# Kernel optimization log

Measured on AMD Instinct MI355X. Metric: run time of the kernel, lower is better.

Reference implementation:

```python
import jax, jax.numpy as jnp
import numpy as np

N, D_IN, UNITS = 8192, 4096, 4096

def ste_sign(k):
    # larq ste_sign forward: sign with sign(0) -> +1
    return jnp.where(k >= 0, 1.0, -1.0).astype(k.dtype)

def setup_inputs() -> dict:
    key = jax.random.key(0)
    kx, kk = jax.random.split(key)
    x = jax.random.normal(kx, (N, D_IN), dtype=jnp.float32)
    kernel = jax.random.normal(kk, (D_IN, UNITS), dtype=jnp.float32)
    return {"x": x, "kernel": kernel}

def reference(x, kernel):
    # y = x @ sign(kernel); the `+ reduce_sum(x)*0` in the original is a no-op
    return x @ ste_sign(kernel)
```

## Files before the change

kernel.cpp:

```cpp
#include <hip/hip_runtime.h>
#include <stdint.h>

typedef __attribute__((ext_vector_type(8))) __bf16 bf16x8;
typedef __attribute__((ext_vector_type(4))) float f32x4;

__device__ inline unsigned short f32_to_bf16_rne(float f) {
  union { float f; uint32_t u; } c; c.f = f;
  uint32_t u = c.u;
  uint32_t r = (u + 0x7FFFu + ((u >> 16) & 1u)) >> 16;
  return (unsigned short)r;
}

__global__ __launch_bounds__(256) void convert_x_kernel(const float* __restrict__ X,
                                                        unsigned short* __restrict__ A,
                                                        size_t n) {
  size_t i = (size_t)blockIdx.x * 256 + threadIdx.x;
  size_t stride = (size_t)gridDim.x * 256;
  for (size_t e = i * 4; e < n; e += stride * 4) {
    const float4 v = *reinterpret_cast<const float4*>(X + e);
    ushort4 o;
    o.x = f32_to_bf16_rne(v.x);
    o.y = f32_to_bf16_rne(v.y);
    o.z = f32_to_bf16_rne(v.z);
    o.w = f32_to_bf16_rne(v.w);
    *reinterpret_cast<ushort4*>(A + e) = o;
  }
}

__global__ __launch_bounds__(256) void sign_transpose_kernel(const float* __restrict__ Km,
                                                             unsigned short* __restrict__ Bt,
                                                             int K, int N) {
  __shared__ unsigned short tile[64][65];
  const int k0 = blockIdx.x * 64;
  const int n0 = blockIdx.y * 64;
  const int t = threadIdx.x;
#pragma unroll
  for (int i = 0; i < 16; ++i) {
    int idx = t + i * 256;
    int kk = idx >> 6, nn = idx & 63;
    float v = Km[(size_t)(k0 + kk) * N + (n0 + nn)];
    tile[kk][nn] = (v >= 0.0f) ? (unsigned short)0x3F80u : (unsigned short)0xBF80u;
  }
  __syncthreads();
#pragma unroll
  for (int i = 0; i < 16; ++i) {
    int idx = t + i * 256;
    int nn = idx >> 6, kk = idx & 63;
    Bt[(size_t)(n0 + nn) * K + (k0 + kk)] = tile[kk][nn];
  }
}


__device__ __forceinline__ void stage_mat(const unsigned short* __restrict__ G,
                                          size_t grow0, int K, int k0,
                                          unsigned short* lds_wave_base,
                                          int tid) {
#pragma unroll
  for (int i = 0; i < 2; ++i) {
    const int row = i * 128 + (tid >> 2);
    const int srcslot = (tid & 3) ^ ((row >> 1) & 3);
    const unsigned short* ga = G + (grow0 + row) * (size_t)K + k0 + srcslot * 8;
    __builtin_amdgcn_global_load_lds(
        (const __attribute__((address_space(1))) void*)ga,
        (__attribute__((address_space(3))) void*)(lds_wave_base + i * 4096),
        16, 0, 0);
  }
}

#define MFMA8(ACCR, AFRAG, BFRAG, I0, I1)                                             \
  __builtin_amdgcn_s_setprio(1);                                                     \
  _Pragma("unroll")                                                                   \
  for (int mi = (I0); mi < (I1); ++mi)                                                \
    _Pragma("unroll")                                                                 \
    for (int ni = 0; ni < 4; ++ni)                                                    \
      acc[(ACCR) + mi][ni] = __builtin_amdgcn_mfma_f32_16x16x32_bf16(                 \
          AFRAG[mi], BFRAG[ni], acc[(ACCR) + mi][ni], 0, 0, 0);                       \
  __builtin_amdgcn_s_setprio(0);                                                      \
  __builtin_amdgcn_sched_barrier(0);

#define GEMM_ITER(T, AFC, BFC, AFN, BFN)                                              \
  {                                                                                   \
    const int cb = ((T) & 3) * 16384;                                                 \
    const int ts = ((T) + 3 < NTt) ? ((T) + 3) : (NTt - 1);                           \
    const int tb = (ts & 3) * 16384;                                                  \
    const int nb = ((T) + 1 < NTt) ? ((((T) + 1) & 3) * 16384) : cb;                  \
    bf16x8 af1[4];                                                                    \
                                                \
    _Pragma("unroll")                                                                 \
    for (int mi = 0; mi < 4; ++mi)                                                    \
      af1[mi] = *reinterpret_cast<const bf16x8*>(&lds[cb + aoff + 2048 + mi * 512]);  \
    stage_mat(A, a_row0, K, ts * 32, &lds[tb + wv * 512], tid);                       \
    __builtin_amdgcn_sched_barrier(0);                                                \
    MFMA8(0, AFC, BFC, 0, 2)                                                          \
                                                       \
    _Pragma("unroll")                                                                 \
    for (int ni = 0; ni < 2; ++ni)                                                    \
      BFN[ni] = *reinterpret_cast<const bf16x8*>(&lds[nb + boff + ni * 512]);         \
    __builtin_amdgcn_sched_barrier(0);                                                \
    MFMA8(0, AFC, BFC, 2, 4)                                                          \
                                \
    _Pragma("unroll")                                                                 \
    for (int ni = 2; ni < 4; ++ni)                                                    \
      BFN[ni] = *reinterpret_cast<const bf16x8*>(&lds[nb + boff + ni * 512]);         \
    _Pragma("unroll")                                                                 \
    for (int mi = 0; mi < 2; ++mi)                                                    \
      AFN[mi] = *reinterpret_cast<const bf16x8*>(&lds[nb + aoff + mi * 512]);         \
    stage_mat(Bt, b_row0, K, ts * 32, &lds[tb + 8192 + wv * 512], tid);               \
    __builtin_amdgcn_sched_barrier(0);                                                \
    MFMA8(4, af1, BFC, 0, 2)                                                          \
                                                       \
    _Pragma("unroll")                                                                 \
    for (int mi = 2; mi < 4; ++mi)                                                    \
      AFN[mi] = *reinterpret_cast<const bf16x8*>(&lds[nb + aoff + mi * 512]);         \
    __builtin_amdgcn_sched_barrier(0);                                                \
    MFMA8(4, af1, BFC, 2, 4)                                                          \
    asm volatile("s_waitcnt vmcnt(4)\n" ::: "memory");                                \
    __builtin_amdgcn_s_barrier();                                                     \
  }

__global__ __launch_bounds__(512, 2) void gemm_bf16_256(const unsigned short* __restrict__ A,
                                                        const unsigned short* __restrict__ Bt,
                                                        float* __restrict__ C,
                                                        int M, int N, int K) {
  __shared__ unsigned short lds[4 * 16384];

  const int nBN = N >> 8;
  const int nwg = gridDim.x;
  const int bid = blockIdx.x;
  int swz = bid;
  if ((nwg & 7) == 0) {
    const int q = nwg >> 3;
    swz = (bid & 7) * q + (bid >> 3);
  }
  const size_t a_row0 = (size_t)(swz / nBN) * 256;
  const size_t b_row0 = (size_t)(swz % nBN) * 256;

  const int tid = threadIdx.x;
  const int wv = tid >> 6, ln = tid & 63;
  const int llo = ln & 15, lhi = ln >> 4;
  const int wr = wv >> 2, wc = wv & 3;
  const int sA = lhi ^ ((llo >> 1) & 3);

  const int aoff = (wr * 128 + llo) * 32 + sA * 8;
  const int boff = 8192 + (wc * 64 + llo) * 32 + sA * 8;

  const int NTt = K >> 5;

  f32x4 acc[8][4];
#pragma unroll
  for (int i = 0; i < 8; ++i)
#pragma unroll
    for (int j = 0; j < 4; ++j) acc[i][j] = (f32x4){0.f, 0.f, 0.f, 0.f};

#pragma unroll
  for (int tt = 0; tt < 3; ++tt) {
    stage_mat(A, a_row0, K, tt * 32, &lds[tt * 16384 + wv * 512], tid);
    stage_mat(Bt, b_row0, K, tt * 32, &lds[tt * 16384 + 8192 + wv * 512], tid);
  }
  asm volatile("s_waitcnt vmcnt(4)\n" ::: "memory");
  __builtin_amdgcn_s_barrier();

  bf16x8 af0_a[4], bfr_a[4], af0_b[4], bfr_b[4];
#pragma unroll
  for (int ni = 0; ni < 4; ++ni)
    bfr_a[ni] = *reinterpret_cast<const bf16x8*>(&lds[boff + ni * 512]);
#pragma unroll
  for (int mi = 0; mi < 4; ++mi)
    af0_a[mi] = *reinterpret_cast<const bf16x8*>(&lds[aoff + mi * 512]);

  for (int t = 0; t < NTt; t += 2) {
    GEMM_ITER(t, af0_a, bfr_a, af0_b, bfr_b)
    GEMM_ITER(t + 1, af0_b, bfr_b, af0_a, bfr_a)
  }

#pragma unroll
  for (int mi = 0; mi < 8; ++mi) {
#pragma unroll
    for (int ni = 0; ni < 4; ++ni) {
      const size_t col = b_row0 + wc * 64 + ni * 16 + llo;
      const size_t rbase = a_row0 + wr * 128 + mi * 16 + lhi * 4;
#pragma unroll
      for (int j = 0; j < 4; ++j)
        C[(rbase + j) * (size_t)N + col] = acc[mi][ni][j];
    }
  }
}

__global__ __launch_bounds__(256) void gemm_f32_fallback(const float* __restrict__ X,
                                                         const float* __restrict__ Km,
                                                         float* __restrict__ C,
                                                         int M, int N, int K) {
  __shared__ float As[64][16];
  __shared__ float Bs[16][65];
  const int nBN = N / 64;
  const int bm = blockIdx.x / nBN;
  const int bn = blockIdx.x % nBN;
  const int t = threadIdx.x;
  const int tx = t & 15, ty = t >> 4;
  float acc[4][4] = {};
  for (int kb = 0; kb < K; kb += 16) {
#pragma unroll
    for (int i = 0; i < 4; ++i) {
      int e = t + i * 256;
      int r = e >> 4, c = e & 15;
      As[r][c] = X[(size_t)(bm * 64 + r) * K + kb + c];
      int rk = e >> 6, cn = e & 63;
      float v = Km[(size_t)(kb + rk) * N + bn * 64 + cn];
      Bs[rk][cn] = (v >= 0.f) ? 1.f : -1.f;
    }
    __syncthreads();
#pragma unroll
    for (int kk = 0; kk < 16; ++kk) {
      float a[4], b[4];
#pragma unroll
      for (int r = 0; r < 4; ++r) a[r] = As[ty * 4 + r][kk];
#pragma unroll
      for (int c = 0; c < 4; ++c) b[c] = Bs[kk][tx * 4 + c];
#pragma unroll
      for (int r = 0; r < 4; ++r)
#pragma unroll
        for (int c = 0; c < 4; ++c) acc[r][c] += a[r] * b[c];
    }
    __syncthreads();
  }
#pragma unroll
  for (int r = 0; r < 4; ++r)
#pragma unroll
    for (int c = 0; c < 4; ++c)
      C[(size_t)(bm * 64 + ty * 4 + r) * N + bn * 64 + tx * 4 + c] = acc[r][c];
}

extern "C" void kernel_launch(void* const* d_in, const int* in_sizes, int n_in,
                              void* d_out, int out_size, void* d_ws, size_t ws_size,
                              hipStream_t stream) {
  const float* x = (const float*)d_in[0];
  const float* kern = (const float*)d_in[1];
  float* out = (float*)d_out;

  const int K = 4096;
  const int N = 4096;
  const int M = in_sizes[0] / K;

  const size_t a_bytes = (size_t)M * K * 2;
  const size_t b_bytes = (size_t)N * K * 2;

  if (ws_size >= a_bytes + b_bytes && (M % 256) == 0 && (N % 256) == 0 && (K % 128) == 0) {
    unsigned short* A = (unsigned short*)d_ws;
    unsigned short* Bt = (unsigned short*)((char*)d_ws + a_bytes);
    convert_x_kernel<<<2048, 256, 0, stream>>>(x, A, (size_t)M * K);
    sign_transpose_kernel<<<dim3(K / 64, N / 64), 256, 0, stream>>>(kern, Bt, K, N);
    gemm_bf16_256<<<(M / 256) * (N / 256), 512, 0, stream>>>(A, Bt, out, M, N, K);
  } else {
    gemm_f32_fallback<<<(M / 64) * (N / 64), 256, 0, stream>>>(x, kern, out, M, N, K);
  }
}
```

Measured before the change: 272.2 us.

## Shrink GEMM tile to 128x256 with 4 waves and triple-buffered LDS

Replaces the 256x256, 8-wave GEMM block with a 128x256, 4-wave block where each wave owns all 128 rows and a 64-column strip. The pipeline drops from a 4-stage to a 3-stage LDS ring with rotating buffer offsets and a prefetch distance of two, and it waits for all loads (vmcnt(0)) at each step. The intent is a smaller LDS footprint and more workgroups for occupancy and load balance. The cost is lower data reuse per block, twice as many blocks re-reading B, and a shallower load overlap.

```diff
diff --git a/kernel.cpp b/kernel.cpp
--- a/kernel.cpp
+++ b/kernel.cpp
@@ -51,24 +51,25 @@
 }
 
 
-__device__ __forceinline__ void stage_mat(const unsigned short* __restrict__ G,
-                                          size_t grow0, int K, int k0,
-                                          unsigned short* lds_wave_base,
-                                          int tid) {
-#pragma unroll
-  for (int i = 0; i < 2; ++i) {
-    const int row = i * 128 + (tid >> 2);
+template <int NISS>
+__device__ __forceinline__ void stage_rows(const unsigned short* __restrict__ G,
+                                           size_t grow0, int K, int k0,
+                                           unsigned short* lds_base,
+                                           int tid) {
+#pragma unroll
+  for (int i = 0; i < NISS; ++i) {
+    const int row = i * 64 + (tid >> 2);
     const int srcslot = (tid & 3) ^ ((row >> 1) & 3);
     const unsigned short* ga = G + (grow0 + row) * (size_t)K + k0 + srcslot * 8;
     __builtin_amdgcn_global_load_lds(
         (const __attribute__((address_space(1))) void*)ga,
-        (__attribute__((address_space(3))) void*)(lds_wave_base + i * 4096),
+        (__attribute__((address_space(3))) void*)(lds_base + i * 2048 + (tid >> 6) * 512),
         16, 0, 0);
   }
 }
 
 #define MFMA8(ACCR, AFRAG, BFRAG, I0, I1)                                             \
-  __builtin_amdgcn_s_setprio(1);                                                     \
+  __builtin_amdgcn_s_setprio(1);                                                      \
   _Pragma("unroll")                                                                   \
   for (int mi = (I0); mi < (I1); ++mi)                                                \
     _Pragma("unroll")                                                                 \
@@ -78,51 +79,44 @@
   __builtin_amdgcn_s_setprio(0);                                                      \
   __builtin_amdgcn_sched_barrier(0);
 
-#define GEMM_ITER(T, AFC, BFC, AFN, BFN)                                              \
+#define GEMM_ITER(T, CBo, NBo, TBo, AFC, BFC, AFN, BFN)                               \
   {                                                                                   \
-    const int cb = ((T) & 3) * 16384;                                                 \
-    const int ts = ((T) + 3 < NTt) ? ((T) + 3) : (NTt - 1);                           \
-    const int tb = (ts & 3) * 16384;                                                  \
-    const int nb = ((T) + 1 < NTt) ? ((((T) + 1) & 3) * 16384) : cb;                  \
+    const int ts = ((T) + 2 < NTt) ? ((T) + 2) : (NTt - 1);                           \
     bf16x8 af1[4];                                                                    \
-                                                \
     _Pragma("unroll")                                                                 \
     for (int mi = 0; mi < 4; ++mi)                                                    \
-      af1[mi] = *reinterpret_cast<const bf16x8*>(&lds[cb + aoff + 2048 + mi * 512]);  \
-    stage_mat(A, a_row0, K, ts * 32, &lds[tb + wv * 512], tid);                       \
+      af1[mi] = *reinterpret_cast<const bf16x8*>(&lds[(CBo) + aoff + 2048 + mi * 512]); \
+    stage_rows<2>(A, a_row0, K, ts * 32, (unsigned short*)lds + (TBo), tid);          \
     __builtin_amdgcn_sched_barrier(0);                                                \
     MFMA8(0, AFC, BFC, 0, 2)                                                          \
-                                                       \
     _Pragma("unroll")                                                                 \
     for (int ni = 0; ni < 2; ++ni)                                                    \
-      BFN[ni] = *reinterpret_cast<const bf16x8*>(&lds[nb + boff + ni * 512]);         \
+      BFN[ni] = *reinterpret_cast<const bf16x8*>(&lds[(NBo) + boff + ni * 512]);      \
     __builtin_amdgcn_sched_barrier(0);                                                \
     MFMA8(0, AFC, BFC, 2, 4)                                                          \
-                                \
     _Pragma("unroll")                                                                 \
     for (int ni = 2; ni < 4; ++ni)                                                    \
-      BFN[ni] = *reinterpret_cast<const bf16x8*>(&lds[nb + boff + ni * 512]);         \
+      BFN[ni] = *reinterpret_cast<const bf16x8*>(&lds[(NBo) + boff + ni * 512]);      \
     _Pragma("unroll")                                                                 \
     for (int mi = 0; mi < 2; ++mi)                                                    \
-      AFN[mi] = *reinterpret_cast<const bf16x8*>(&lds[nb + aoff + mi * 512]);         \
-    stage_mat(Bt, b_row0, K, ts * 32, &lds[tb + 8192 + wv * 512], tid);               \
+      AFN[mi] = *reinterpret_cast<const bf16x8*>(&lds[(NBo) + aoff + mi * 512]);      \
+    stage_rows<4>(Bt, b_row0, K, ts * 32, (unsigned short*)lds + (TBo) + 4096, tid);  \
     __builtin_amdgcn_sched_barrier(0);                                                \
     MFMA8(4, af1, BFC, 0, 2)                                                          \
-                                                       \
     _Pragma("unroll")                                                                 \
     for (int mi = 2; mi < 4; ++mi)                                                    \
-      AFN[mi] = *reinterpret_cast<const bf16x8*>(&lds[nb + aoff + mi * 512]);         \
+      AFN[mi] = *reinterpret_cast<const bf16x8*>(&lds[(NBo) + aoff + mi * 512]);      \
     __builtin_amdgcn_sched_barrier(0);                                                \
     MFMA8(4, af1, BFC, 2, 4)                                                          \
-    asm volatile("s_waitcnt vmcnt(4)\n" ::: "memory");                                \
+    asm volatile("s_waitcnt vmcnt(0)\n" ::: "memory");                                \
     __builtin_amdgcn_s_barrier();                                                     \
   }
 
-__global__ __launch_bounds__(512, 2) void gemm_bf16_256(const unsigned short* __restrict__ A,
-                                                        const unsigned short* __restrict__ Bt,
-                                                        float* __restrict__ C,
-                                                        int M, int N, int K) {
-  __shared__ unsigned short lds[4 * 16384];
+__global__ __launch_bounds__(256, 2) void gemm_bf16_128x256(const unsigned short* __restrict__ A,
+                                                            const unsigned short* __restrict__ Bt,
+                                                            float* __restrict__ C,
+                                                            int M, int N, int K) {
+  __shared__ unsigned short lds[3 * 12288];
 
   const int nBN = N >> 8;
   const int nwg = gridDim.x;
@@ -132,17 +126,17 @@
     const int q = nwg >> 3;
     swz = (bid & 7) * q + (bid >> 3);
   }
-  const size_t a_row0 = (size_t)(swz / nBN) * 256;
+  const size_t a_row0 = (size_t)(swz / nBN) * 128;
   const size_t b_row0 = (size_t)(swz % nBN) * 256;
 
   const int tid = threadIdx.x;
   const int wv = tid >> 6, ln = tid & 63;
   const int llo = ln & 15, lhi = ln >> 4;
-  const int wr = wv >> 2, wc = wv & 3;
+  const int wc = wv;
   const int sA = lhi ^ ((llo >> 1) & 3);
 
-  const int aoff = (wr * 128 + llo) * 32 + sA * 8;
-  const int boff = 8192 + (wc * 64 + llo) * 32 + sA * 8;
+  const int aoff = llo * 32 + sA * 8;
+  const int boff = 4096 + (wc * 64 + llo) * 32 + sA * 8;
 
   const int NTt = K >> 5;
 
@@ -152,12 +146,11 @@
 #pragma unroll
     for (int j = 0; j < 4; ++j) acc[i][j] = (f32x4){0.f, 0.f, 0.f, 0.f};
 
-#pragma unroll
-  for (int tt = 0; tt < 3; ++tt) {
-    stage_mat(A, a_row0, K, tt * 32, &lds[tt * 16384 + wv * 512], tid);
-    stage_mat(Bt, b_row0, K, tt * 32, &lds[tt * 16384 + 8192 + wv * 512], tid);
-  }
-  asm volatile("s_waitcnt vmcnt(4)\n" ::: "memory");
+  stage_rows<2>(A, a_row0, K, 0, (unsigned short*)lds, tid);
+  stage_rows<4>(Bt, b_row0, K, 0, (unsigned short*)lds + 4096, tid);
+  stage_rows<2>(A, a_row0, K, 32, (unsigned short*)lds + 12288, tid);
+  stage_rows<4>(Bt, b_row0, K, 32, (unsigned short*)lds + 12288 + 4096, tid);
+  asm volatile("s_waitcnt vmcnt(0)\n" ::: "memory");
   __builtin_amdgcn_s_barrier();
 
   bf16x8 af0_a[4], bfr_a[4], af0_b[4], bfr_b[4];
@@ -168,9 +161,12 @@
   for (int mi = 0; mi < 4; ++mi)
     af0_a[mi] = *reinterpret_cast<const bf16x8*>(&lds[aoff + mi * 512]);
 
+  int cb = 0, nb2 = 12288, tb = 24576;
   for (int t = 0; t < NTt; t += 2) {
-    GEMM_ITER(t, af0_a, bfr_a, af0_b, bfr_b)
-    GEMM_ITER(t + 1, af0_b, bfr_b, af0_a, bfr_a)
+    GEMM_ITER(t, cb, nb2, tb, af0_a, bfr_a, af0_b, bfr_b)
+    { int tmp = cb; cb = nb2; nb2 = tb; tb = tmp; }
+    GEMM_ITER(t + 1, cb, nb2, tb, af0_b, bfr_b, af0_a, bfr_a)
+    { int tmp = cb; cb = nb2; nb2 = tb; tb = tmp; }
   }
 
 #pragma unroll
@@ -178,7 +174,7 @@
 #pragma unroll
     for (int ni = 0; ni < 4; ++ni) {
       const size_t col = b_row0 + wc * 64 + ni * 16 + llo;
-      const size_t rbase = a_row0 + wr * 128 + mi * 16 + lhi * 4;
+      const size_t rbase = a_row0 + mi * 16 + lhi * 4;
 #pragma unroll
       for (int j = 0; j < 4; ++j)
         C[(rbase + j) * (size_t)N + col] = acc[mi][ni][j];
@@ -244,12 +240,12 @@
   const size_t a_bytes = (size_t)M * K * 2;
   const size_t b_bytes = (size_t)N * K * 2;
 
-  if (ws_size >= a_bytes + b_bytes && (M % 256) == 0 && (N % 256) == 0 && (K % 128) == 0) {
+  if (ws_size >= a_bytes + b_bytes && (M % 128) == 0 && (N % 256) == 0 && (K % 128) == 0) {
     unsigned short* A = (unsigned short*)d_ws;
     unsigned short* Bt = (unsigned short*)((char*)d_ws + a_bytes);
     convert_x_kernel<<<2048, 256, 0, stream>>>(x, A, (size_t)M * K);
     sign_transpose_kernel<<<dim3(K / 64, N / 64), 256, 0, stream>>>(kern, Bt, K, N);
-    gemm_bf16_256<<<(M / 256) * (N / 256), 512, 0, stream>>>(A, Bt, out, M, N, K);
+    gemm_bf16_128x256<<<(M / 128) * (N / 256), 256, 0, stream>>>(A, Bt, out, M, N, K);
   } else {
     gemm_f32_fallback<<<(M / 64) * (N / 64), 256, 0, stream>>>(x, kern, out, M, N, K);
   }
```

Measured after the change: 301.7 us. 10.8% more time.
